# Kernel optimization log

Measured on AMD Instinct MI355X. Metric: run time of the kernel, lower is better.

## Reference

```python
import jax, jax.numpy as jnp
import numpy as np

QLEN, MLEN, BSZ = 1024, 1024, 4
D_MODEL, N_HEAD, D_HEAD, D_INNER = 1024, 16, 64, 4096
KLEN = QLEN + MLEN  # = rlen
LN_EPS = 1e-5


def setup_inputs() -> dict:
    key = jax.random.key(0)
    ks = jax.random.split(key, 16)
    s = 0.02
    nhd = N_HEAD * D_HEAD
    inp = {
        "dec_inp": jax.random.normal(ks[0], (QLEN, BSZ, D_MODEL), jnp.float32),
        "r": jax.random.normal(ks[1], (KLEN, D_MODEL), jnp.float32),
        "r_w_bias": jax.random.normal(ks[2], (N_HEAD, D_HEAD), jnp.float32) * s,
        "r_r_bias": jax.random.normal(ks[3], (N_HEAD, D_HEAD), jnp.float32) * s,
        "mems": jax.random.normal(ks[4], (MLEN, BSZ, D_MODEL), jnp.float32),
        # causal mask with memory: position j visible to query i iff j <= i + MLEN
        "dec_attn_mask": (jnp.arange(KLEN)[None, :] > (jnp.arange(QLEN)[:, None] + MLEN))[:, :, None],
        # parameters
        "qkv_w": jax.random.normal(ks[5], (D_MODEL, 3 * nhd), jnp.float32) * s,
        "r_w": jax.random.normal(ks[6], (D_MODEL, nhd), jnp.float32) * s,
        "o_w": jax.random.normal(ks[7], (nhd, D_MODEL), jnp.float32) * s,
        "ln1_w": jnp.ones((D_MODEL,), jnp.float32),
        "ln1_b": jnp.zeros((D_MODEL,), jnp.float32),
        "ln2_w": jnp.ones((D_MODEL,), jnp.float32),
        "ln2_b": jnp.zeros((D_MODEL,), jnp.float32),
        "ff_w1": jax.random.normal(ks[8], (D_MODEL, D_INNER), jnp.float32) * s,
        "ff_b1": jnp.zeros((D_INNER,), jnp.float32),
        "ff_w2": jax.random.normal(ks[9], (D_INNER, D_MODEL), jnp.float32) * s,
        "ff_b2": jnp.zeros((D_MODEL,), jnp.float32),
    }
    return inp


def _layer_norm(x, w, b):
    mu = jnp.mean(x, axis=-1, keepdims=True)
    var = jnp.mean(jnp.square(x - mu), axis=-1, keepdims=True)
    return (x - mu) * jax.lax.rsqrt(var + LN_EPS) * w + b


def _rel_shift(x):
    # x: [qlen, rlen, bsz, n_head] -- Transformer-XL pad/reshape shift
    q, rl = x.shape[0], x.shape[1]
    zero_pad = jnp.zeros((q, 1) + x.shape[2:], x.dtype)
    x_padded = jnp.concatenate([zero_pad, x], axis=1)
    x_padded = x_padded.reshape((rl + 1, q) + x.shape[2:])
    return x_padded[1:].reshape(x.shape)


def reference(dec_inp, r, r_w_bias, r_r_bias, mems, dec_attn_mask,
              qkv_w, r_w, o_w, ln1_w, ln1_b, ln2_w, ln2_b,
              ff_w1, ff_b1, ff_w2, ff_b2):
    qlen, bsz = dec_inp.shape[0], dec_inp.shape[1]
    nhd = N_HEAD * D_HEAD
    scale = 1.0 / (D_HEAD ** 0.5)

    cat = jnp.concatenate([mems, dec_inp], axis=0)          # [klen, b, d]
    w_heads = cat @ qkv_w                                   # [klen, b, 3*nhd]
    w_head_q, w_head_k, w_head_v = jnp.split(w_heads, 3, axis=-1)
    w_head_q = w_head_q[-qlen:]                             # [qlen, b, nhd]
    klen = w_head_k.shape[0]

    w_head_q = w_head_q.reshape(qlen, bsz, N_HEAD, D_HEAD)
    w_head_k = w_head_k.reshape(klen, bsz, N_HEAD, D_HEAD)
    w_head_v = w_head_v.reshape(klen, bsz, N_HEAD, D_HEAD)
    r_head_k = (r @ r_w).reshape(-1, N_HEAD, D_HEAD)        # [rlen, n, d]

    AC = jnp.einsum('ibnd,jbnd->ijbn', w_head_q + r_w_bias, w_head_k)
    BD = jnp.einsum('ibnd,jnd->ijbn', w_head_q + r_r_bias, r_head_k)
    BD = _rel_shift(BD)

    attn_score = (AC + BD) * scale                          # [q, k, b, n]
    attn_score = jnp.where(dec_attn_mask[:, :, :, None], -jnp.inf, attn_score)
    attn_prob = jax.nn.softmax(attn_score, axis=1)

    attn_vec = jnp.einsum('ijbn,jbnd->ibnd', attn_prob, w_head_v)
    attn_out = attn_vec.reshape(qlen, bsz, nhd) @ o_w       # [q, b, d]

    output = _layer_norm(dec_inp + attn_out, ln1_w, ln1_b)
    ff = jax.nn.relu(output @ ff_w1 + ff_b1) @ ff_w2 + ff_b2
    return _layer_norm(output + ff, ln2_w, ln2_b)
```

## Files before the change

### kernel.cpp

```cpp
#include <hip/hip_runtime.h>
#include <hip/hip_bf16.h>
#include <math.h>

#define QLEN 1024
#define MLEN 1024
#define BSZ 4
#define KLEN 2048
#define NH 16
#define DH 64
#define DM 1024
#define DI 4096
#define NHD 1024
#define LN_EPS 1e-5f

typedef short bf16x8 __attribute__((ext_vector_type(8)));
typedef float f32x4 __attribute__((ext_vector_type(4)));
typedef unsigned int uint4v __attribute__((ext_vector_type(4)));

__device__ __forceinline__ float bf2f(unsigned short u) {
    union { unsigned u32; float f; } x; x.u32 = ((unsigned)u) << 16; return x.f;
}
__device__ __forceinline__ unsigned short f2bf(float f) {
    __hip_bfloat16 h = __float2bfloat16(f);
    return *(unsigned short*)&h;
}

static const size_t OFF_CATB  = 0;
static const size_t OFF_VTG   = 0;
static const size_t OFF_WHB   = 16777216;
static const size_t OFF_RB    = 67108864;
static const size_t OFF_RHKB  = 71303168;
static const size_t OFF_AVB   = 75497472;
static const size_t OFF_TMP   = 83886080;
static const size_t OFF_LN1F  = 100663296;
static const size_t OFF_LN1B  = 117440512;
static const size_t OFF_FFHB  = 125829120;
static const size_t OFF_QKVWT = 159383552;
static const size_t OFF_RWT   = 165675008;
static const size_t OFF_OWT   = 167772160;
static const size_t OFF_FFW1T = 169869312;
static const size_t OFF_FFW2T = 178257920;

__global__ __launch_bounds__(256) void cast_cat(const float* __restrict__ mems,
                                                const float* __restrict__ dec,
                                                unsigned short* __restrict__ out) {
    size_t i8 = ((size_t)blockIdx.x * 256 + threadIdx.x) * 8;
    const size_t half = (size_t)MLEN * BSZ * DM;
    const float* src = (i8 < half) ? (mems + i8) : (dec + (i8 - half));
    float4 v0 = *(const float4*)src;
    float4 v1 = *(const float4*)(src + 4);
    ushort4 o0 = {f2bf(v0.x), f2bf(v0.y), f2bf(v0.z), f2bf(v0.w)};
    ushort4 o1 = {f2bf(v1.x), f2bf(v1.y), f2bf(v1.z), f2bf(v1.w)};
    *(ushort4*)&out[i8] = o0;
    *(ushort4*)&out[i8 + 4] = o1;
}

__global__ __launch_bounds__(256) void cast_f32_bf16(const float* __restrict__ in,
                                                     unsigned short* __restrict__ out) {
    size_t i8 = ((size_t)blockIdx.x * 256 + threadIdx.x) * 8;
    float4 v0 = *(const float4*)(in + i8);
    float4 v1 = *(const float4*)(in + i8 + 4);
    ushort4 o0 = {f2bf(v0.x), f2bf(v0.y), f2bf(v0.z), f2bf(v0.w)};
    ushort4 o1 = {f2bf(v1.x), f2bf(v1.y), f2bf(v1.z), f2bf(v1.w)};
    *(ushort4*)&out[i8] = o0;
    *(ushort4*)&out[i8 + 4] = o1;
}

__global__ __launch_bounds__(256) void transpose_cast_all(
        const float* __restrict__ qkv_w, const float* __restrict__ r_w,
        const float* __restrict__ o_w,  const float* __restrict__ ff_w1,
        const float* __restrict__ ff_w2,
        unsigned short* __restrict__ qkvwT, unsigned short* __restrict__ rwT,
        unsigned short* __restrict__ owT, unsigned short* __restrict__ ffw1T,
        unsigned short* __restrict__ ffw2T) {
    __shared__ float tile[32][33];
    const int bid = blockIdx.x;
    const float* in; unsigned short* out; int K, N, nx, lid;
    if (bid < 3072)      { in = qkv_w; out = qkvwT; K = 1024; N = 3072; nx = 96;  lid = bid; }
    else if (bid < 4096) { in = r_w;   out = rwT;   K = 1024; N = 1024; nx = 32;  lid = bid - 3072; }
    else if (bid < 5120) { in = o_w;   out = owT;   K = 1024; N = 1024; nx = 32;  lid = bid - 4096; }
    else if (bid < 9216) { in = ff_w1; out = ffw1T; K = 1024; N = 4096; nx = 128; lid = bid - 5120; }
    else                 { in = ff_w2; out = ffw2T; K = 4096; N = 1024; nx = 32;  lid = bid - 9216; }
    const int n0 = (lid % nx) * 32;
    const int k0 = (lid / nx) * 32;
    const int t = threadIdx.x;
    const int r = t >> 3;
    const int c0 = (t & 7) << 2;
    float4 v = *(const float4*)&in[(size_t)(k0 + r) * N + n0 + c0];
    tile[r][c0 + 0] = v.x; tile[r][c0 + 1] = v.y;
    tile[r][c0 + 2] = v.z; tile[r][c0 + 3] = v.w;
    __syncthreads();
    ushort4 o = {f2bf(tile[c0 + 0][r]), f2bf(tile[c0 + 1][r]),
                 f2bf(tile[c0 + 2][r]), f2bf(tile[c0 + 3][r])};
    *(ushort4*)&out[(size_t)(n0 + r) * K + k0 + c0] = o;
}

__global__ __launch_bounds__(256) void gemm_bf16(const unsigned short* __restrict__ A,
                                                 const unsigned short* __restrict__ Bt,
                                                 const float* __restrict__ bias,
                                                 void* __restrict__ C,
                                                 int M, int N, int K, int flags) {
    __shared__ __align__(16) unsigned short As[128 * 64];
    __shared__ __align__(16) unsigned short Bs[128 * 64];

    const int tid = threadIdx.x;
    const int w = tid >> 6, l = tid & 63;
    const int wr = w >> 1, wc = w & 1;
    const int row0 = blockIdx.y * 128;
    const int col0 = blockIdx.x * 128;

    f32x4 acc[4][4] = {};

    uint4v ra[4], rb[4];
    {
#pragma unroll
        for (int q = 0; q < 4; ++q) {
            int f = q * 256 + tid, r = f >> 3, c = f & 7;
            ra[q] = *(const uint4v*)&A[(size_t)(row0 + r) * K + c * 8];
            rb[q] = *(const uint4v*)&Bt[(size_t)(col0 + r) * K + c * 8];
        }
    }

    const int nt = K >> 6;
    for (int kt = 0; kt < nt; ++kt) {
        __syncthreads();
#pragma unroll
        for (int q = 0; q < 4; ++q) {
            int f = q * 256 + tid, r = f >> 3, c = f & 7;
            int sw = (c ^ (r & 7)) << 3;
            *(uint4v*)&As[r * 64 + sw] = ra[q];
            *(uint4v*)&Bs[r * 64 + sw] = rb[q];
        }
        __syncthreads();
        if (kt + 1 < nt) {
            const int k0 = (kt + 1) << 6;
#pragma unroll
            for (int q = 0; q < 4; ++q) {
                int f = q * 256 + tid, r = f >> 3, c = f & 7;
                ra[q] = *(const uint4v*)&A[(size_t)(row0 + r) * K + k0 + c * 8];
                rb[q] = *(const uint4v*)&Bt[(size_t)(col0 + r) * K + k0 + c * 8];
            }
        }
#pragma unroll
        for (int ks = 0; ks < 2; ++ks) {
            bf16x8 a[4], bfr[4];
#pragma unroll
            for (int m = 0; m < 4; ++m) {
                int arow = wr * 64 + m * 16 + (l & 15);
                int chunk = (ks * 4 + (l >> 4)) ^ (arow & 7);
                a[m] = *(const bf16x8*)&As[arow * 64 + chunk * 8];
            }
#pragma unroll
            for (int n = 0; n < 4; ++n) {
                int brow = wc * 64 + n * 16 + (l & 15);
                int chunk = (ks * 4 + (l >> 4)) ^ (brow & 7);
                bfr[n] = *(const bf16x8*)&Bs[brow * 64 + chunk * 8];
            }
#pragma unroll
            for (int m = 0; m < 4; ++m)
#pragma unroll
                for (int n = 0; n < 4; ++n)
                    acc[m][n] = __builtin_amdgcn_mfma_f32_16x16x32_bf16(a[m], bfr[n], acc[m][n], 0, 0, 0);
        }
    }

#pragma unroll
    for (int n = 0; n < 4; ++n) {
        const int ccol = col0 + wc * 64 + n * 16 + (l & 15);
        const float bv = (flags & 1) ? bias[ccol] : 0.0f;
#pragma unroll
        for (int m = 0; m < 4; ++m) {
            const int crow0 = row0 + wr * 64 + m * 16 + ((l >> 4) << 2);
#pragma unroll
            for (int reg = 0; reg < 4; ++reg) {
                float v = acc[m][n][reg] + bv;
                if (flags & 2) v = fmaxf(v, 0.0f);
                if (flags & 4)
                    ((unsigned short*)C)[(size_t)(crow0 + reg) * N + ccol] = f2bf(v);
                else
                    ((float*)C)[(size_t)(crow0 + reg) * N + ccol] = v;
            }
        }
    }
}

__global__ __launch_bounds__(256) void vtrans(const unsigned short* __restrict__ whb,
                                              unsigned short* __restrict__ vtg) {
    __shared__ unsigned short tile[64][72];
    const int bn = blockIdx.y;
    const int b = bn >> 4, n = bn & 15, nb = n * 64;
    const int jt0 = blockIdx.x * 64;
    const int tid = threadIdx.x;
#pragma unroll
    for (int g = 0; g < 2; ++g) {
        int f = g * 256 + tid;
        int key = f >> 3, c = f & 7;
        uint4v v = *(const uint4v*)&whb[((size_t)(jt0 + key) * 4 + b) * 3072 + 2048 + nb + c * 8];
        *(uint4v*)&tile[key][c * 8] = v;
    }
    __syncthreads();
#pragma unroll
    for (int g = 0; g < 2; ++g) {
        int f = g * 256 + tid;
        int d = f >> 3, ck = f & 7;
        unsigned short tmp[8];
#pragma unroll
        for (int e = 0; e < 8; ++e) tmp[e] = tile[ck * 8 + e][d];
        *(uint4v*)&vtg[(size_t)bn * 131072 + (size_t)d * 2048 + jt0 + ck * 8] = *(uint4v*)tmp;
    }
}

__global__ __launch_bounds__(512) void flash_attn_mfma(const unsigned short* __restrict__ whb,
                                                       const unsigned short* __restrict__ rhkb,
                                                       const unsigned short* __restrict__ vtg,
                                                       const float* __restrict__ r_w_bias,
                                                       const float* __restrict__ r_r_bias,
                                                       unsigned short* __restrict__ avb) {
    const int bid = blockIdx.x;
    const int bn = bid >> 3;
    const int z = bid & 7;
    const int bx = (z & 1) ? (z >> 1) : 7 - (z >> 1);
    const int b = bn >> 4, n = bn & 15, nb = n * 64;
    const int i0 = bx << 7;
    const int tid = threadIdx.x;
    const int wq = tid >> 6;
    const int lane = tid & 63;
    const int rg = lane >> 4;
    const int lc = lane & 15;
    const int m7 = lc & 7;

    __shared__ __align__(16) unsigned short Ks[4096];
    __shared__ __align__(16) unsigned short Rs[16384];
    __shared__ __align__(16) unsigned short Vt[4096];
    __shared__ __align__(16) unsigned short SCR[8][1280];

    bf16x8 qac0, qac1, qbd0, qbd1;
    {
        const int qrow = MLEN + i0 + wq * 16 + lc;
        const unsigned short* qp = whb + ((size_t)qrow * 4 + b) * 3072 + nb + rg * 8;
        bf16x8 q0 = *(const bf16x8*)(qp);
        bf16x8 q1 = *(const bf16x8*)(qp + 32);
        const float* wbp = r_w_bias + nb + rg * 8;
        const float* rbp = r_r_bias + nb + rg * 8;
#pragma unroll
        for (int e = 0; e < 8; ++e) {
            const float v0 = bf2f((unsigned short)q0[e]);
            const float v1 = bf2f((unsigned short)q1[e]);
            qac0[e] = (short)f2bf((v0 + wbp[e]) * 0.125f);
            qbd0[e] = (short)f2bf((v0 + rbp[e]) * 0.125f);
            qac1[e] = (short)f2bf((v1 + wbp[32 + e]) * 0.125f);
            qbd1[e] = (short)f2bf((v1 + rbp[32 + e]) * 0.125f);
        }
    }

    f32x4 Oacc[4] = {};
    float mrun = -INFINITY, lrun = 0.f;

    const int ntiles = 2 * bx + 18;
    const int wbase_off = 112 - 16 * wq;

    const int srow = tid >> 3;
    const int sc = tid & 7;
    unsigned short* scr = &SCR[wq][0];

    uint4v pk, pv, pr3[3];
    {
        pk = *(const uint4v*)&whb[((size_t)srow * 4 + b) * 3072 + 1024 + nb + sc * 8];
        pv = *(const uint4v*)&vtg[(size_t)bn * 131072 + (size_t)srow * 2048 + sc * 8];
        const int relbase0 = 896 - i0;
#pragma unroll
        for (int p = 0; p < 3; ++p) {
            const int a = relbase0 + p * 64 + srow;
            pr3[p] = *(const uint4v*)&rhkb[(size_t)a * 1024 + nb + sc * 8];
        }
    }

    for (int kt = 0; kt < ntiles; ++kt) {
        const int jt0 = kt << 6;
        const int relbase = jt0 - i0 + 896;
        __syncthreads();

        *(uint4v*)&Ks[srow * 64 + ((sc ^ (srow & 7)) << 3)] = pk;
        *(uint4v*)&Vt[srow * 64 + ((sc ^ (srow & 7)) << 3)] = pv;
        if (kt == 0) {
#pragma unroll
            for (int p = 0; p < 3; ++p) {
                const int a = relbase + p * 64 + srow;
                const int dst = ((a >> 6) & 3) * 4096 + (a & 63) * 64 + ((sc ^ (a & 7)) << 3);
                *(uint4v*)&Rs[dst] = pr3[p];
            }
        } else {
            const int a = relbase + 128 + srow;
            const int dst = ((a >> 6) & 3) * 4096 + (a & 63) * 64 + ((sc ^ (a & 7)) << 3);
            *(uint4v*)&Rs[dst] = pr3[0];
        }
        if (kt + 1 < ntiles) {
            const int jn = jt0 + 64;
            pk = *(const uint4v*)&whb[((size_t)(jn + srow) * 4 + b) * 3072 + 1024 + nb + sc * 8];
            pv = *(const uint4v*)&vtg[(size_t)bn * 131072 + (size_t)srow * 2048 + jn + sc * 8];
            int a = relbase + 192 + srow;
            if (a > 2047) a = 2047;
            pr3[0] = *(const uint4v*)&rhkb[(size_t)a * 1024 + nb + sc * 8];
        }
        __syncthreads();

        f32x4 S[4];
        __builtin_amdgcn_s_setprio(1);
#pragma unroll
        for (int nf = 0; nf < 4; ++nf) {
            const int row = nf * 16 + lc;
            const bf16x8 kf0 = *(const bf16x8*)&Ks[row * 64 + ((rg ^ m7) << 3)];
            const bf16x8 kf1 = *(const bf16x8*)&Ks[row * 64 + (((4 + rg) ^ m7) << 3)];
            f32x4 zz = {0.f, 0.f, 0.f, 0.f};
            zz = __builtin_amdgcn_mfma_f32_16x16x32_bf16(kf0, qac0, zz, 0, 0, 0);
            S[nf] = __builtin_amdgcn_mfma_f32_16x16x32_bf16(kf1, qac1, zz, 0, 0, 0);
        }
        __builtin_amdgcn_s_setprio(0);

        const int wbase = relbase + wbase_off;
#pragma unroll
        for (int g = 0; g < 5; ++g) {
            const int a = wbase + g * 16 + lc;
            const int rbase = ((a >> 6) & 3) * 4096 + (a & 63) * 64;
            const bf16x8 rf0 = *(const bf16x8*)&Rs[rbase + ((rg ^ m7) << 3)];
            const bf16x8 rf1 = *(const bf16x8*)&Rs[rbase + (((4 + rg) ^ m7) << 3)];
            f32x4 bd = {0.f, 0.f, 0.f, 0.f};
            bd = __builtin_amdgcn_mfma_f32_16x16x32_bf16(rf0, qbd0, bd, 0, 0, 0);
            bd = __builtin_amdgcn_mfma_f32_16x16x32_bf16(rf1, qbd1, bd, 0, 0, 0);
            ushort4 p4 = {f2bf(bd[0]), f2bf(bd[1]), f2bf(bd[2]), f2bf(bd[3])};
            *(ushort4*)&scr[lc * 80 + g * 16 + rg * 4] = p4;
        }

        const bool needmask = (wbase + 78 > 2047);
        float tmax = -INFINITY;
#pragma unroll
        for (int nf = 0; nf < 4; ++nf) {
#pragma unroll
            for (int r = 0; r < 4; ++r) {
                const int wb_ = 15 + nf * 16 + rg * 4 + r - lc;
                float s = S[nf][r] + bf2f(scr[lc * 80 + wb_]);
                if (needmask) s = (wbase + wb_ <= 2047) ? s : -INFINITY;
                S[nf][r] = s;
                tmax = fmaxf(tmax, s);
            }
        }

        tmax = fmaxf(tmax, __shfl_xor(tmax, 16));
        tmax = fmaxf(tmax, __shfl_xor(tmax, 32));
        const float mn = fmaxf(mrun, tmax);
        const float ef = __expf(mrun - mn);
        mrun = mn;
        float rsum = 0.f;
#pragma unroll
        for (int nf = 0; nf < 4; ++nf) {
#pragma unroll
            for (int r = 0; r < 4; ++r) {
                const float p = __expf(S[nf][r] - mn);
                S[nf][r] = p;
                rsum += p;
            }
        }
        rsum += __shfl_xor(rsum, 16);
        rsum += __shfl_xor(rsum, 32);
        lrun = lrun * ef + rsum;
        if (__any(ef < 1.0f)) {
#pragma unroll
            for (int nf = 0; nf < 4; ++nf)
#pragma unroll
                for (int r = 0; r < 4; ++r) Oacc[nf][r] *= ef;
        }

#pragma unroll
        for (int nf = 0; nf < 4; ++nf) {
            ushort4 pw = {f2bf(S[nf][0]), f2bf(S[nf][1]), f2bf(S[nf][2]), f2bf(S[nf][3])};
            const int chunk = nf * 2 + (rg >> 1);
            *(ushort4*)&scr[lc * 80 + ((chunk ^ m7) << 3) + ((rg & 1) << 2)] = pw;
        }

        {
            const bf16x8 pf0 = *(const bf16x8*)&scr[lc * 80 + ((rg ^ m7) << 3)];
            const bf16x8 pf1 = *(const bf16x8*)&scr[lc * 80 + (((4 + rg) ^ m7) << 3)];
            __builtin_amdgcn_s_setprio(1);
#pragma unroll
            for (int nf = 0; nf < 4; ++nf) {
                const int row = nf * 16 + lc;
                const bf16x8 vf0 = *(const bf16x8*)&Vt[row * 64 + ((rg ^ m7) << 3)];
                const bf16x8 vf1 = *(const bf16x8*)&Vt[row * 64 + (((4 + rg) ^ m7) << 3)];
                Oacc[nf] = __builtin_amdgcn_mfma_f32_16x16x32_bf16(vf0, pf0, Oacc[nf], 0, 0, 0);
                Oacc[nf] = __builtin_amdgcn_mfma_f32_16x16x32_bf16(vf1, pf1, Oacc[nf], 0, 0, 0);
            }
            __builtin_amdgcn_s_setprio(0);
        }
    }

    const float inv = 1.0f / lrun;
    const int qg = i0 + wq * 16 + lc;
#pragma unroll
    for (int nf = 0; nf < 4; ++nf) {
        ushort4 o = {f2bf(Oacc[nf][0] * inv), f2bf(Oacc[nf][1] * inv),
                     f2bf(Oacc[nf][2] * inv), f2bf(Oacc[nf][3] * inv)};
        *(ushort4*)&avb[((size_t)qg * 4 + b) * 1024 + nb + nf * 16 + rg * 4] = o;
    }
}

__global__ __launch_bounds__(256) void add_ln_kernel(const float* __restrict__ a,
                                                     const float* __restrict__ b,
                                                     const float* __restrict__ w,
                                                     const float* __restrict__ bias,
                                                     float* __restrict__ out,
                                                     unsigned short* __restrict__ out_bf) {
    const int row = blockIdx.x;
    const int t = threadIdx.x;
    __shared__ float xs[DM];
    __shared__ float red[256];

    const float* ar = a + (size_t)row * DM;
    const float* br = b + (size_t)row * DM;

    float lsum = 0.f;
#pragma unroll
    for (int c = t; c < DM; c += 256) {
        float v = ar[c] + br[c];
        xs[c] = v;
        lsum += v;
    }
    red[t] = lsum;
    __syncthreads();
    for (int off = 128; off > 0; off >>= 1) {
        if (t < off) red[t] += red[t + off];
        __syncthreads();
    }
    const float mu = red[0] * (1.0f / DM);
    __syncthreads();

    float lvar = 0.f;
#pragma unroll
    for (int c = t; c < DM; c += 256) {
        float dv = xs[c] - mu;
        lvar += dv * dv;
    }
    red[t] = lvar;
    __syncthreads();
    for (int off = 128; off > 0; off >>= 1) {
        if (t < off) red[t] += red[t + off];
        __syncthreads();
    }
    const float rstd = rsqrtf(red[0] * (1.0f / DM) + LN_EPS);
    __syncthreads();

    float* orow = out + (size_t)row * DM;
#pragma unroll
    for (int c = t; c < DM; c += 256) {
        float v = (xs[c] - mu) * rstd * w[c] + bias[c];
        orow[c] = v;
        if (out_bf) out_bf[(size_t)row * DM + c] = f2bf(v);
    }
}

extern "C" void kernel_launch(void* const* d_in, const int* in_sizes, int n_in,
                              void* d_out, int out_size, void* d_ws, size_t ws_size,
                              hipStream_t stream) {
    const float* dec_inp  = (const float*)d_in[0];
    const float* r        = (const float*)d_in[1];
    const float* r_w_bias = (const float*)d_in[2];
    const float* r_r_bias = (const float*)d_in[3];
    const float* mems     = (const float*)d_in[4];
    const float* qkv_w    = (const float*)d_in[6];
    const float* r_w      = (const float*)d_in[7];
    const float* o_w      = (const float*)d_in[8];
    const float* ln1_w    = (const float*)d_in[9];
    const float* ln1_b    = (const float*)d_in[10];
    const float* ln2_w    = (const float*)d_in[11];
    const float* ln2_b    = (const float*)d_in[12];
    const float* ff_w1    = (const float*)d_in[13];
    const float* ff_b1    = (const float*)d_in[14];
    const float* ff_w2    = (const float*)d_in[15];
    const float* ff_b2    = (const float*)d_in[16];
    float* out = (float*)d_out;
    char* ws = (char*)d_ws;

    unsigned short* catb  = (unsigned short*)(ws + OFF_CATB);
    unsigned short* vtg   = (unsigned short*)(ws + OFF_VTG);
    unsigned short* whb   = (unsigned short*)(ws + OFF_WHB);
    unsigned short* rb    = (unsigned short*)(ws + OFF_RB);
    unsigned short* rhkb  = (unsigned short*)(ws + OFF_RHKB);
    unsigned short* avb   = (unsigned short*)(ws + OFF_AVB);
    float*          tmp   = (float*)(ws + OFF_TMP);
    float*          ln1f  = (float*)(ws + OFF_LN1F);
    unsigned short* ln1b  = (unsigned short*)(ws + OFF_LN1B);
    unsigned short* ffhb  = (unsigned short*)(ws + OFF_FFHB);
    unsigned short* qkvwT = (unsigned short*)(ws + OFF_QKVWT);
    unsigned short* rwT   = (unsigned short*)(ws + OFF_RWT);
    unsigned short* owT   = (unsigned short*)(ws + OFF_OWT);
    unsigned short* ffw1T = (unsigned short*)(ws + OFF_FFW1T);
    unsigned short* ffw2T = (unsigned short*)(ws + OFF_FFW2T);

    cast_cat<<<dim3(4096), 256, 0, stream>>>(mems, dec_inp, catb);
    cast_f32_bf16<<<dim3(1024), 256, 0, stream>>>(r, rb);
    transpose_cast_all<<<dim3(13312), 256, 0, stream>>>(
        qkv_w, r_w, o_w, ff_w1, ff_w2, qkvwT, rwT, owT, ffw1T, ffw2T);

    gemm_bf16<<<dim3(24, 64), 256, 0, stream>>>(catb, qkvwT, nullptr, whb,
                                                KLEN * BSZ, 3 * NHD, DM, 4);
    gemm_bf16<<<dim3(8, 16), 256, 0, stream>>>(rb, rwT, nullptr, rhkb,
                                               KLEN, NHD, DM, 4);

    vtrans<<<dim3(32, 64), 256, 0, stream>>>(whb, vtg);

    flash_attn_mfma<<<dim3(512), 512, 0, stream>>>(
        whb, rhkb, vtg, r_w_bias, r_r_bias, avb);

    gemm_bf16<<<dim3(8, 32), 256, 0, stream>>>(avb, owT, nullptr, tmp,
                                               QLEN * BSZ, DM, NHD, 0);
    add_ln_kernel<<<dim3(QLEN * BSZ), 256, 0, stream>>>(
        dec_inp, tmp, ln1_w, ln1_b, ln1f, ln1b);
    gemm_bf16<<<dim3(32, 32), 256, 0, stream>>>(ln1b, ffw1T, ff_b1, ffhb,
                                                QLEN * BSZ, DI, DM, 1 | 2 | 4);
    gemm_bf16<<<dim3(8, 32), 256, 0, stream>>>(ffhb, ffw2T, ff_b2, tmp,
                                               QLEN * BSZ, DM, DI, 1);
    add_ln_kernel<<<dim3(QLEN * BSZ), 256, 0, stream>>>(
        ln1f, tmp, ln2_w, ln2_b, out, nullptr);
}
```

Measured before the change: 421.7 us.

## Use direct global-to-LDS loads with double buffering in GEMM, pad scratch, vectorize LayerNorm

The GEMM now uses global_load_lds to stream tiles straight into a double-buffered shared memory layout, replacing the register-staged copy. This cuts VGPR pressure and one sync per iteration. The XOR swizzle on LDS reads is dropped, which may bring back bank conflicts. Separately, the attention scratch row stride is padded from 80 to 88 to reduce bank conflicts. The add+LayerNorm kernel is rewritten with float4 vector loads and stores held in registers instead of a shared buffer.

```diff
diff --git a/kernel.cpp b/kernel.cpp
--- a/kernel.cpp
+++ b/kernel.cpp
@@ -23,6 +23,10 @@
 __device__ __forceinline__ unsigned short f2bf(float f) {
     __hip_bfloat16 h = __float2bfloat16(f);
     return *(unsigned short*)&h;
+}
+__device__ __forceinline__ void gload16(const void* g, void* l) {
+    __builtin_amdgcn_global_load_lds((const __attribute__((address_space(1))) unsigned int*)g,
+                                     (__attribute__((address_space(3))) unsigned int*)l, 16, 0, 0);
 }
 
 static const size_t OFF_CATB  = 0;
@@ -100,45 +104,37 @@
                                                  const float* __restrict__ bias,
                                                  void* __restrict__ C,
                                                  int M, int N, int K, int flags) {
-    __shared__ __align__(16) unsigned short As[128 * 64];
-    __shared__ __align__(16) unsigned short Bs[128 * 64];
+    __shared__ __align__(16) unsigned short As[2][128 * 64];
+    __shared__ __align__(16) unsigned short Bs[2][128 * 64];
 
     const int tid = threadIdx.x;
     const int w = tid >> 6, l = tid & 63;
     const int wr = w >> 1, wc = w & 1;
     const int row0 = blockIdx.y * 128;
     const int col0 = blockIdx.x * 128;
+    const int r32 = tid >> 3;
+    const int c8 = tid & 7;
 
     f32x4 acc[4][4] = {};
-
-    uint4v ra[4], rb[4];
-    {
-#pragma unroll
-        for (int q = 0; q < 4; ++q) {
-            int f = q * 256 + tid, r = f >> 3, c = f & 7;
-            ra[q] = *(const uint4v*)&A[(size_t)(row0 + r) * K + c * 8];
-            rb[q] = *(const uint4v*)&Bt[(size_t)(col0 + r) * K + c * 8];
-        }
-    }
-
     const int nt = K >> 6;
+
+#pragma unroll
+    for (int q = 0; q < 4; ++q) {
+        const int row = q * 32 + r32;
+        gload16(&A[(size_t)(row0 + row) * K + c8 * 8], &As[0][row * 64 + c8 * 8]);
+        gload16(&Bt[(size_t)(col0 + row) * K + c8 * 8], &Bs[0][row * 64 + c8 * 8]);
+    }
+    __syncthreads();
+
+    int cur = 0;
     for (int kt = 0; kt < nt; ++kt) {
-        __syncthreads();
-#pragma unroll
-        for (int q = 0; q < 4; ++q) {
-            int f = q * 256 + tid, r = f >> 3, c = f & 7;
-            int sw = (c ^ (r & 7)) << 3;
-            *(uint4v*)&As[r * 64 + sw] = ra[q];
-            *(uint4v*)&Bs[r * 64 + sw] = rb[q];
-        }
-        __syncthreads();
         if (kt + 1 < nt) {
             const int k0 = (kt + 1) << 6;
 #pragma unroll
             for (int q = 0; q < 4; ++q) {
-                int f = q * 256 + tid, r = f >> 3, c = f & 7;
-                ra[q] = *(const uint4v*)&A[(size_t)(row0 + r) * K + k0 + c * 8];
-                rb[q] = *(const uint4v*)&Bt[(size_t)(col0 + r) * K + k0 + c * 8];
+                const int row = q * 32 + r32;
+                gload16(&A[(size_t)(row0 + row) * K + k0 + c8 * 8], &As[cur ^ 1][row * 64 + c8 * 8]);
+                gload16(&Bt[(size_t)(col0 + row) * K + k0 + c8 * 8], &Bs[cur ^ 1][row * 64 + c8 * 8]);
             }
         }
 #pragma unroll
@@ -146,15 +142,13 @@
             bf16x8 a[4], bfr[4];
 #pragma unroll
             for (int m = 0; m < 4; ++m) {
-                int arow = wr * 64 + m * 16 + (l & 15);
-                int chunk = (ks * 4 + (l >> 4)) ^ (arow & 7);
-                a[m] = *(const bf16x8*)&As[arow * 64 + chunk * 8];
+                const int arow = wr * 64 + m * 16 + (l & 15);
+                a[m] = *(const bf16x8*)&As[cur][arow * 64 + ks * 32 + (l >> 4) * 8];
             }
 #pragma unroll
             for (int n = 0; n < 4; ++n) {
-                int brow = wc * 64 + n * 16 + (l & 15);
-                int chunk = (ks * 4 + (l >> 4)) ^ (brow & 7);
-                bfr[n] = *(const bf16x8*)&Bs[brow * 64 + chunk * 8];
+                const int brow = wc * 64 + n * 16 + (l & 15);
+                bfr[n] = *(const bf16x8*)&Bs[cur][brow * 64 + ks * 32 + (l >> 4) * 8];
             }
 #pragma unroll
             for (int m = 0; m < 4; ++m)
@@ -162,6 +156,8 @@
                 for (int n = 0; n < 4; ++n)
                     acc[m][n] = __builtin_amdgcn_mfma_f32_16x16x32_bf16(a[m], bfr[n], acc[m][n], 0, 0, 0);
         }
+        __syncthreads();
+        cur ^= 1;
     }
 
 #pragma unroll
@@ -232,7 +228,7 @@
     __shared__ __align__(16) unsigned short Ks[4096];
     __shared__ __align__(16) unsigned short Rs[16384];
     __shared__ __align__(16) unsigned short Vt[4096];
-    __shared__ __align__(16) unsigned short SCR[8][1280];
+    __shared__ __align__(16) unsigned short SCR[8][1408];
 
     bf16x8 qac0, qac1, qbd0, qbd1;
     {
@@ -328,7 +324,7 @@
             bd = __builtin_amdgcn_mfma_f32_16x16x32_bf16(rf0, qbd0, bd, 0, 0, 0);
             bd = __builtin_amdgcn_mfma_f32_16x16x32_bf16(rf1, qbd1, bd, 0, 0, 0);
             ushort4 p4 = {f2bf(bd[0]), f2bf(bd[1]), f2bf(bd[2]), f2bf(bd[3])};
-            *(ushort4*)&scr[lc * 80 + g * 16 + rg * 4] = p4;
+            *(ushort4*)&scr[lc * 88 + g * 16 + rg * 4] = p4;
         }
 
         const bool needmask = (wbase + 78 > 2047);
@@ -338,7 +334,7 @@
 #pragma unroll
             for (int r = 0; r < 4; ++r) {
                 const int wb_ = 15 + nf * 16 + rg * 4 + r - lc;
-                float s = S[nf][r] + bf2f(scr[lc * 80 + wb_]);
+                float s = S[nf][r] + bf2f(scr[lc * 88 + wb_]);
                 if (needmask) s = (wbase + wb_ <= 2047) ? s : -INFINITY;
                 S[nf][r] = s;
                 tmax = fmaxf(tmax, s);
@@ -374,12 +370,12 @@
         for (int nf = 0; nf < 4; ++nf) {
             ushort4 pw = {f2bf(S[nf][0]), f2bf(S[nf][1]), f2bf(S[nf][2]), f2bf(S[nf][3])};
             const int chunk = nf * 2 + (rg >> 1);
-            *(ushort4*)&scr[lc * 80 + ((chunk ^ m7) << 3) + ((rg & 1) << 2)] = pw;
+            *(ushort4*)&scr[lc * 88 + ((chunk ^ m7) << 3) + ((rg & 1) << 2)] = pw;
         }
 
         {
-            const bf16x8 pf0 = *(const bf16x8*)&scr[lc * 80 + ((rg ^ m7) << 3)];
-            const bf16x8 pf1 = *(const bf16x8*)&scr[lc * 80 + (((4 + rg) ^ m7) << 3)];
+            const bf16x8 pf0 = *(const bf16x8*)&scr[lc * 88 + ((rg ^ m7) << 3)];
+            const bf16x8 pf1 = *(const bf16x8*)&scr[lc * 88 + (((4 + rg) ^ m7) << 3)];
             __builtin_amdgcn_s_setprio(1);
 #pragma unroll
             for (int nf = 0; nf < 4; ++nf) {
@@ -411,20 +407,14 @@
                                                      unsigned short* __restrict__ out_bf) {
     const int row = blockIdx.x;
     const int t = threadIdx.x;
-    __shared__ float xs[DM];
+    const int c0 = t << 2;
     __shared__ float red[256];
 
-    const float* ar = a + (size_t)row * DM;
-    const float* br = b + (size_t)row * DM;
-
-    float lsum = 0.f;
-#pragma unroll
-    for (int c = t; c < DM; c += 256) {
-        float v = ar[c] + br[c];
-        xs[c] = v;
-        lsum += v;
-    }
-    red[t] = lsum;
+    const float4 av = *(const float4*)&a[(size_t)row * DM + c0];
+    const float4 bv = *(const float4*)&b[(size_t)row * DM + c0];
+    float x0 = av.x + bv.x, x1 = av.y + bv.y, x2 = av.z + bv.z, x3 = av.w + bv.w;
+
+    red[t] = x0 + x1 + x2 + x3;
     __syncthreads();
     for (int off = 128; off > 0; off >>= 1) {
         if (t < off) red[t] += red[t + off];
@@ -433,27 +423,23 @@
     const float mu = red[0] * (1.0f / DM);
     __syncthreads();
 
-    float lvar = 0.f;
-#pragma unroll
-    for (int c = t; c < DM; c += 256) {
-        float dv = xs[c] - mu;
-        lvar += dv * dv;
-    }
-    red[t] = lvar;
+    const float d0 = x0 - mu, d1 = x1 - mu, d2 = x2 - mu, d3 = x3 - mu;
+    red[t] = d0 * d0 + d1 * d1 + d2 * d2 + d3 * d3;
     __syncthreads();
     for (int off = 128; off > 0; off >>= 1) {
         if (t < off) red[t] += red[t + off];
         __syncthreads();
     }
     const float rstd = rsqrtf(red[0] * (1.0f / DM) + LN_EPS);
-    __syncthreads();
-
-    float* orow = out + (size_t)row * DM;
-#pragma unroll
-    for (int c = t; c < DM; c += 256) {
-        float v = (xs[c] - mu) * rstd * w[c] + bias[c];
-        orow[c] = v;
-        if (out_bf) out_bf[(size_t)row * DM + c] = f2bf(v);
+
+    const float4 wv = *(const float4*)&w[c0];
+    const float4 bsv = *(const float4*)&bias[c0];
+    float4 o = {d0 * rstd * wv.x + bsv.x, d1 * rstd * wv.y + bsv.y,
+                d2 * rstd * wv.z + bsv.z, d3 * rstd * wv.w + bsv.w};
+    *(float4*)&out[(size_t)row * DM + c0] = o;
+    if (out_bf) {
+        ushort4 ob = {f2bf(o.x), f2bf(o.y), f2bf(o.z), f2bf(o.w)};
+        *(ushort4*)&out_bf[(size_t)row * DM + c0] = ob;
     }
 }
 
```

Result: slower. 484.0 us (+14.8%).
